# Performance work log

Measured on AMD Instinct MI355X. Metric: run time of the kernel, lower is better.

The kernel has to match this reference:

```python
import jax, jax.numpy as jnp
import numpy as np

B = 1024      # number of states
NP = 32       # SVGD particles per state
AD = 20       # act_dim
OD = 64       # obs_dim
H = 256       # critic hidden width
STEPS = 5     # num_svgd_steps
LR = 0.1      # svgd_lr (adaptive_lr disabled)
SP0 = 1.0     # svgd_sigma_p0
ALIM = 1.0    # act_limit


def _q(obs, X, w1, b1, w2, b2, w3, b3):
    h = jnp.concatenate([obs, X], axis=-1)
    h = jax.nn.relu(h @ w1 + b1)
    h = jax.nn.relu(h @ w2 + b2)
    return jnp.squeeze(h @ w3 + b3, -1)


def _rbf(X):
    # X: [B, NP, AD] -> K [B,NP,NP], diff [B,NP,NP,AD], gamma [B,1,1], K_grad [B,NP,NP,AD]
    diff = X[:, :, None, :] - X[:, None, :, :]
    dist_sq = jnp.sum(diff * diff, axis=-1)
    # adaptive bandwidth via median heuristic (adaptive_sig=True)
    med = jnp.median(dist_sq.reshape(dist_sq.shape[0], -1), axis=-1)
    sig_sq = med / (2.0 * jnp.log(NP + 1.0))
    gamma = (1.0 / (2.0 * sig_sq + 1e-8))[:, None, None]
    K = jnp.exp(-gamma * dist_sq)
    K_grad = -2.0 * gamma[..., None] * diff * K[..., None]  # d/dx_i K(x_i, x_j)
    return K, diff, gamma, K_grad


def setup_inputs():
    key = jax.random.key(0)
    ks = jax.random.split(key, 16)
    N = B * NP

    def lin(k, fi, fo):
        return (jax.random.normal(k, (fi, fo), jnp.float32) / np.sqrt(fi)).astype(jnp.float32)

    return {
        "obs": jax.random.normal(ks[0], (N, OD), jnp.float32),
        "a0": jax.random.normal(ks[1], (N, AD), jnp.float32) * np.sqrt(SP0),
        "q1_w1": lin(ks[2], OD + AD, H), "q1_b1": jnp.zeros((H,), jnp.float32),
        "q1_w2": lin(ks[3], H, H),       "q1_b2": jnp.zeros((H,), jnp.float32),
        "q1_w3": lin(ks[4], H, 1),       "q1_b3": jnp.zeros((1,), jnp.float32),
        "q2_w1": lin(ks[5], OD + AD, H), "q2_b1": jnp.zeros((H,), jnp.float32),
        "q2_w2": lin(ks[6], H, H),       "q2_b2": jnp.zeros((H,), jnp.float32),
        "q2_w3": lin(ks[7], H, 1),       "q2_b3": jnp.zeros((1,), jnp.float32),
    }


def reference(obs, a0, q1_w1, q1_b1, q1_w2, q1_b2, q1_w3, q1_b3,
              q2_w1, q2_b1, q2_w2, q2_b2, q2_w3, q2_b3):
    eye = jnp.eye(NP, dtype=a0.dtype)

    def q_min_sum(Xf):
        q1 = _q(obs, Xf, q1_w1, q1_b1, q1_w2, q1_b2, q1_w3, q1_b3)
        q2 = _q(obs, Xf, q2_w1, q2_b1, q2_w2, q2_b2, q2_w3, q2_b3)
        return jnp.sum(jnp.minimum(q1, q2))

    score_fn = jax.grad(q_min_sum)  # autograd score function

    def step(carry, _):
        a, logp = carry
        score = score_fn(a).reshape(-1, NP, AD)                 # [B,NP,AD]
        X = a.reshape(-1, NP, AD)
        K, diff, gamma, Kg = _rbf(X)
        phi = (jnp.einsum('bij,bjd->bid', K, score) + Kg.sum(axis=1)) / NP
        # log-prob correction terms (with_logprob=True)
        term1 = jnp.mean(jnp.sum(Kg * score[:, None, :, :], axis=-1), axis=2)     # [B,NP]
        inner = jnp.sum(jnp.transpose(Kg, (0, 2, 1, 3)) * diff, axis=-1) \
                - AD * (K - eye)
        term2 = -2.0 * gamma[:, :, 0] * jnp.mean(inner, axis=1)                   # [B,NP]
        logp = logp - LR * (term1 + term2)
        a = a + LR * phi.reshape(a.shape)                        # svgd_optim
        return (a, logp), None

    logp0 = jnp.zeros((B, NP), a0.dtype)
    (a, logp_svgd), _ = jax.lax.scan(step, (a0, logp0), None, length=STEPS)

    a_sq = ALIM * jnp.tanh(a)                                    # [B*NP, AD]
    logp_normal = (-AD * 0.5 * jnp.log(2.0 * jnp.pi * SP0)
                   - 0.5 / SP0 * jnp.sum(a0 * a0, axis=-1)).reshape(-1, NP)
    logp_tanh = -jnp.sum(2.0 * (jnp.log(2.0) - a - jax.nn.softplus(-2.0 * a)),
                         axis=-1).reshape(-1, NP)
    logp_a = jnp.mean(logp_normal + logp_svgd + logp_tanh, axis=-1)  # [B]
    return a_sq, logp_a
```

## Files before the change

### kernel.cpp

```cpp
#include <hip/hip_runtime.h>
#include <math.h>

#define NPART 32
#define ADIM  20
#define ODIM  64
#define HID   256
#define NSTEPS 5
#define LRC   0.1f
#define NBLK  512
#define LOG33 3.4965075614664802f

typedef short bf8 __attribute__((ext_vector_type(8)));
typedef float f4  __attribute__((ext_vector_type(4)));

#define OW1T(n) ((n)*24576)
#define OW2T(n) (49152 + (n)*65536)
#define OW2C(n) (180224 + (n)*65536)
#define OW1X(n) (311296 + (n)*8192)
#define OW3B(n) (327680 + (n)*256)
#define WS_ELEMS 328192

__device__ __forceinline__ short f2bf(float x) {
    unsigned u = __float_as_uint(x);
    u += 0x7FFFu + ((u >> 16) & 1u);
    return (short)(u >> 16);
}
__device__ __forceinline__ short f2bfT(float x) {
    return (short)(__float_as_uint(x) >> 16);
}
__device__ __forceinline__ float bf2f(short s) {
    return __uint_as_float(((unsigned)(unsigned short)s) << 16);
}

#define MFMA(a,b,c) __builtin_amdgcn_mfma_f32_16x16x32_bf16((a),(b),(c),0,0,0)

__global__ void prep_weights(const float* __restrict__ w1a, const float* __restrict__ w2a,
                             const float* __restrict__ w3a, const float* __restrict__ w1b,
                             const float* __restrict__ w2b, const float* __restrict__ w3b,
                             unsigned short* __restrict__ ws)
{
    int idx = blockIdx.x * 256 + threadIdx.x;
    if (idx >= WS_ELEMS) return;
    float val;
    if (idx < 49152) {
        int net = idx / 24576, rem = idx % 24576;
        int n = rem / 96, k = rem % 96;
        const float* w1 = net ? w1b : w1a;
        val = (k < 84) ? w1[k*256 + n] : 0.f;
    } else if (idx < 180224) {
        int t2 = idx - 49152; int net = t2 / 65536, rem = t2 % 65536;
        int n = rem / 256, k = rem % 256;
        const float* w2 = net ? w2b : w2a;
        val = w2[k*256 + n];
    } else if (idx < 311296) {
        int t2 = idx - 180224; int net = t2 / 65536, rem = t2 % 65536;
        const float* w2 = net ? w2b : w2a;
        val = w2[rem];
    } else if (idx < 327680) {
        int t2 = idx - 311296; int net = t2 / 8192, rem = t2 % 8192;
        int d = rem / 256, n = rem % 256;
        const float* w1 = net ? w1b : w1a;
        val = (d < 20) ? w1[(64 + d)*256 + n] : 0.f;
    } else {
        int t2 = idx - 327680; int net = t2 / 256, k = t2 % 256;
        const float* w3 = net ? w3b : w3a;
        val = w3[k];
    }
    ws[idx] = (unsigned short)f2bf(val);
}

__global__ void __launch_bounds__(512, 4)
svgd_main(const float* __restrict__ obs,  const float* __restrict__ a0g,
          const float* __restrict__ b1a,  const float* __restrict__ b2a, const float* __restrict__ b3a,
          const float* __restrict__ b1b,  const float* __restrict__ b2b, const float* __restrict__ b3b,
          const float* __restrict__ w3af, const float* __restrict__ w3bf,
          const unsigned short* __restrict__ ws, float* __restrict__ out)
{
    __shared__ __align__(16) short A0s[64*96];
    __shared__ __align__(16) short hbuf[64*264];
    __shared__ unsigned maskS[2][2][64][8];
    __shared__ float Xm[64*20];
    __shared__ float scoreS[64*21];
    __shared__ float qpart[2][8][64];
    __shared__ int   winsS[64];
    __shared__ float logps[64];
    __shared__ unsigned short lutI[496], lutJ[496];
    __shared__ float med2[4];
    __shared__ float qvS[64];
    __shared__ float normsS[64], diagS[64], rowKS[64];

    float* d2sF = (float*)hbuf;
    float* GSF  = ((float*)hbuf) + 2048;
    short* KbS  = hbuf + 8192;
    short* SBs  = hbuf + 10240;
    short* STbS = hbuf + 12288;
    short* XTbS = hbuf + 14336;

    const int t = threadIdx.x, b = blockIdx.x;
    const int lane = t & 63, wv = t >> 6;
    const int q = lane >> 4, mp = lane & 15;
    const int nb = wv * 32;

    for (int p = t; p < 64*ODIM; p += 512) {
        int i = p >> 6, d = p & 63;
        A0s[i*96 + d] = f2bfT(obs[(b*64 + i)*ODIM + d]);
    }
    for (int p = t; p < 64*ADIM; p += 512) {
        int i = p / 20, d = p - i*20;
        float v = a0g[(b*64 + i)*20 + d];
        Xm[p] = v;
        A0s[i*96 + 64 + d] = f2bfT(v);
    }
    for (int p = t; p < 64*12; p += 512) { int i = p/12, d = p - i*12; A0s[i*96 + 84 + d] = 0; }
    { unsigned* mz = &maskS[0][0][0][0];
      for (int p = t; p < 2*2*64*8; p += 512) mz[p] = 0u; }
    if (t < 496) {
        int i_ = 0, rem = t;
        while (rem >= 31 - i_) { rem -= 31 - i_; ++i_; }
        lutI[t] = (unsigned short)i_; lutJ[t] = (unsigned short)(i_ + 1 + rem);
    }
    if (t < 64) logps[t] = 0.f;
    __syncthreads();

    for (int step = 0; step < NSTEPS; ++step) {
        for (int net = 0; net < 2; ++net) {
            const unsigned short* w1t = ws + OW1T(net);
            const unsigned short* w2t = ws + OW2T(net);
            const float* b1p = net ? b1b : b1a;
            const float* b2p = net ? b2b : b2a;
            const float* w3p = net ? w3bf : w3af;

            f4 acc[4][2];
            #pragma unroll
            for (int h = 0; h < 4; ++h) { acc[h][0] = (f4){0,0,0,0}; acc[h][1] = (f4){0,0,0,0}; }
            {
                const unsigned short* bp0 = w1t + (size_t)(nb +      mp)*96 + q*8;
                const unsigned short* bp1 = w1t + (size_t)(nb + 16 + mp)*96 + q*8;
                bf8 bb0 = *(const bf8*)bp0, bb1 = *(const bf8*)bp1;
                #pragma unroll
                for (int k0 = 0; k0 < 96; k0 += 32) {
                    bf8 n0 = bb0, n1 = bb1;
                    if (k0 + 32 < 96) { n0 = *(const bf8*)(bp0 + k0 + 32); n1 = *(const bf8*)(bp1 + k0 + 32); }
                    #pragma unroll
                    for (int h = 0; h < 4; ++h) {
                        bf8 aa = *(const bf8*)&A0s[(h*16 + mp)*96 + k0 + q*8];
                        acc[h][0] = MFMA(aa, bb0, acc[h][0]);
                        acc[h][1] = MFMA(aa, bb1, acc[h][1]);
                    }
                    bb0 = n0; bb1 = n1;
                }
            }
            #pragma unroll
            for (int h = 0; h < 4; ++h) {
                #pragma unroll
                for (int s = 0; s < 2; ++s) {
                    int n0 = nb + s*16, col = n0 + mp;
                    float bias = b1p[col];
                    #pragma unroll
                    for (int r = 0; r < 4; ++r) {
                        float v = acc[h][s][r] + bias;
                        bool pos = v > 0.f;
                        unsigned long long bal = __ballot(pos);
                        hbuf[(h*16 + q*4 + r)*264 + col] = f2bfT(pos ? v : 0.f);
                        if (mp == 0)
                            atomicOr(&maskS[net][0][h*16 + q*4 + r][n0 >> 5],
                                     ((unsigned)((bal >> (q*16)) & 0xFFFFull)) << (n0 & 16));
                    }
                }
            }
            __syncthreads();

            #pragma unroll
            for (int h = 0; h < 4; ++h) { acc[h][0] = (f4){0,0,0,0}; acc[h][1] = (f4){0,0,0,0}; }
            {
                const unsigned short* bp0 = w2t + (size_t)(nb +      mp)*256 + q*8;
                const unsigned short* bp1 = w2t + (size_t)(nb + 16 + mp)*256 + q*8;
                bf8 bb0 = *(const bf8*)bp0, bb1 = *(const bf8*)bp1;
                #pragma unroll
                for (int k0 = 0; k0 < 256; k0 += 32) {
                    bf8 n0 = bb0, n1 = bb1;
                    if (k0 + 32 < 256) { n0 = *(const bf8*)(bp0 + k0 + 32); n1 = *(const bf8*)(bp1 + k0 + 32); }
                    #pragma unroll
                    for (int h = 0; h < 4; ++h) {
                        bf8 aa = *(const bf8*)&hbuf[(h*16 + mp)*264 + k0 + q*8];
                        acc[h][0] = MFMA(aa, bb0, acc[h][0]);
                        acc[h][1] = MFMA(aa, bb1, acc[h][1]);
                    }
                    bb0 = n0; bb1 = n1;
                }
            }
            {
                float qp[4][4] = {{0,0,0,0},{0,0,0,0},{0,0,0,0},{0,0,0,0}};
                #pragma unroll
                for (int h = 0; h < 4; ++h) {
                    #pragma unroll
                    for (int s = 0; s < 2; ++s) {
                        int n0 = nb + s*16, col = n0 + mp;
                        float bias = b2p[col], w3v = w3p[col];
                        #pragma unroll
                        for (int r = 0; r < 4; ++r) {
                            float v = acc[h][s][r] + bias;
                            bool pos = v > 0.f;
                            unsigned long long bal = __ballot(pos);
                            if (mp == 0)
                                atomicOr(&maskS[net][1][h*16 + q*4 + r][n0 >> 5],
                                         ((unsigned)((bal >> (q*16)) & 0xFFFFull)) << (n0 & 16));
                            qp[h][r] += pos ? v * w3v : 0.f;
                        }
                    }
                }
                #pragma unroll
                for (int d = 1; d < 16; d <<= 1)
                    #pragma unroll
                    for (int h = 0; h < 4; ++h)
                        #pragma unroll
                        for (int r = 0; r < 4; ++r)
                            qp[h][r] += __shfl_xor(qp[h][r], d, 64);
                if (mp == 0) {
                    #pragma unroll
                    for (int h = 0; h < 4; ++h)
                        #pragma unroll
                        for (int r = 0; r < 4; ++r)
                            qpart[net][wv][h*16 + q*4 + r] = qp[h][r];
                }
            }
            __syncthreads();
        }

        if (t < 64) {
            float q0 = b3a[0], q1 = b3b[0];
            #pragma unroll
            for (int w = 0; w < 8; ++w) { q0 += qpart[0][w][t]; q1 += qpart[1][w][t]; }
            winsS[t] = (q0 <= q1) ? 0 : 1;
        }
        __syncthreads();

        for (int net = 0; net < 2; ++net) {
            const unsigned short* w2c  = ws + OW2C(net);
            const unsigned short* w3b8 = ws + OW3B(net);

            f4 acc[4][2];
            #pragma unroll
            for (int h = 0; h < 4; ++h) { acc[h][0] = (f4){0,0,0,0}; acc[h][1] = (f4){0,0,0,0}; }
            int win[4];
            #pragma unroll
            for (int h = 0; h < 4; ++h) win[h] = (winsS[h*16 + mp] == net);
            {
                const unsigned short* bp0 = w2c + (size_t)(nb +      mp)*256 + q*8;
                const unsigned short* bp1 = w2c + (size_t)(nb + 16 + mp)*256 + q*8;
                bf8 bb0 = *(const bf8*)bp0, bb1 = *(const bf8*)bp1;
                #pragma unroll
                for (int k0 = 0; k0 < 256; k0 += 32) {
                    bf8 n0 = bb0, n1 = bb1;
                    if (k0 + 32 < 256) { n0 = *(const bf8*)(bp0 + k0 + 32); n1 = *(const bf8*)(bp1 + k0 + 32); }
                    bf8 w3v = *(const bf8*)(w3b8 + k0 + q*8);
                    #pragma unroll
                    for (int h = 0; h < 4; ++h) {
                        unsigned bits = win[h] ? ((maskS[net][1][h*16 + mp][k0 >> 5] >> (q*8)) & 0xFFu) : 0u;
                        bf8 aa;
                        #pragma unroll
                        for (int j = 0; j < 8; ++j)
                            aa[j] = ((bits >> j) & 1u) ? w3v[j] : (short)0;
                        acc[h][0] = MFMA(aa, bb0, acc[h][0]);
                        acc[h][1] = MFMA(aa, bb1, acc[h][1]);
                    }
                    bb0 = n0; bb1 = n1;
                }
            }
            #pragma unroll
            for (int h = 0; h < 4; ++h) {
                #pragma unroll
                for (int s = 0; s < 2; ++s) {
                    int col = nb + s*16 + mp;
                    #pragma unroll
                    for (int r = 0; r < 4; ++r) {
                        int row = h*16 + q*4 + r;
                        bool on = (maskS[net][0][row][col >> 5] >> (col & 31)) & 1u;
                        hbuf[row*264 + col] = f2bfT(on ? acc[h][s][r] : 0.f);
                    }
                }
            }
            __syncthreads();
            {
                int mt = wv & 3, ch = wv >> 2;
                const unsigned short* w1x = ws + OW1X(net);
                const unsigned short* bp  = w1x + (size_t)(ch*16 + mp)*256 + q*8;
                f4 sa = (f4){0,0,0,0};
                bf8 bx = *(const bf8*)bp;
                #pragma unroll
                for (int k0 = 0; k0 < 256; k0 += 32) {
                    bf8 nx = bx;
                    if (k0 + 32 < 256) nx = *(const bf8*)(bp + k0 + 32);
                    bf8 aa = *(const bf8*)&hbuf[(mt*16 + mp)*264 + k0 + q*8];
                    sa = MFMA(aa, bx, sa);
                    bx = nx;
                }
                int colD = ch*16 + mp;
                if (colD < 20) {
                    #pragma unroll
                    for (int r = 0; r < 4; ++r) {
                        int row = mt*16 + q*4 + r;
                        if (net == 0) scoreS[row*21 + colD]  = sa[r];
                        else          scoreS[row*21 + colD] += sa[r];
                    }
                }
            }
            __syncthreads();
        }

        if (t < 64) {
            int st = t >> 5;
            float nrm = 0.f, dg = 0.f;
            #pragma unroll
            for (int d = 0; d < 20; ++d) {
                float xb = bf2f(A0s[t*96 + 64 + d]);
                nrm += xb * xb;
                float sv = scoreS[t*21 + d];
                float xv = Xm[t*20 + d];
                dg += xv * sv;
                short sb = f2bfT(sv);
                SBs[t*32 + d] = sb;
                STbS[st*1024 + d*32 + (t & 31)] = sb;
                XTbS[st*1024 + d*32 + (t & 31)] = f2bfT(xv);
            }
            #pragma unroll
            for (int d = 20; d < 32; ++d) SBs[t*32 + d] = 0;
            normsS[t] = nrm;
            diagS[t]  = dg;
        }
        __syncthreads();

        {
            int stw = wv >> 2, mt = (wv >> 1) & 1, nt = wv & 1;
            bf8 aa  = *(const bf8*)&A0s[(stw*32 + mt*16 + mp)*96 + 64 + q*8];
            bf8 bbx = *(const bf8*)&A0s[(stw*32 + nt*16 + mp)*96 + 64 + q*8];
            bf8 bbs = *(const bf8*)&SBs[(stw*32 + nt*16 + mp)*32 + q*8];
            f4 gx = MFMA(aa, bbx, ((f4){0,0,0,0}));
            f4 gs = MFMA(aa, bbs, ((f4){0,0,0,0}));
            int jl = nt*16 + mp;
            float nj = normsS[stw*32 + jl];
            #pragma unroll
            for (int r = 0; r < 4; ++r) {
                int il = mt*16 + q*4 + r;
                d2sF[stw*1024 + il*32 + jl] = normsS[stw*32 + il] + nj - 2.f*gx[r];
                GSF [stw*1024 + il*32 + jl] = gs[r];
            }
        }
        __syncthreads();

        if (wv < 2) {
            const float* base = d2sF + wv*1024;
            float v[8];
            #pragma unroll
            for (int i = 0; i < 8; ++i) {
                int e = lane*8 + i;
                v[i] = (e < 496) ? base[lutI[e]*32 + lutJ[e]] : 3.4e38f;
            }
            for (int k = 2; k <= 512; k <<= 1) {
                for (int jj = k >> 1; jj >= 8; jj >>= 1) {
                    int lm = jj >> 3;
                    #pragma unroll
                    for (int i = 0; i < 8; ++i) {
                        float w = __shfl_xor(v[i], lm, 64);
                        int p = lane*8 + i;
                        bool takeMin = (((p & k) == 0) == ((p & jj) == 0));
                        v[i] = takeMin ? fminf(v[i], w) : fmaxf(v[i], w);
                    }
                }
                int jj0 = (k >> 1) < 4 ? (k >> 1) : 4;
                for (int jj = jj0; jj >= 1; jj >>= 1) {
                    #pragma unroll
                    for (int i = 0; i < 8; ++i) {
                        if ((i & jj) == 0) {
                            int i2 = i | jj;
                            int p = lane*8 + i;
                            bool up = ((p & k) == 0);
                            float x = v[i], y = v[i2];
                            float mn = fminf(x, y), mx = fmaxf(x, y);
                            v[i] = up ? mn : mx; v[i2] = up ? mx : mn;
                        }
                    }
                }
            }
            if (lane == 29) med2[wv*2 + 0] = v[7];
            if (lane == 30) med2[wv*2 + 1] = v[0];
        } else {
            unsigned* mz = &maskS[0][0][0][0];
            for (int p = t - 128; p < 2*2*64*8; p += 384) mz[p] = 0u;
        }
        __syncthreads();

        {
            int i = t >> 3, stw = i >> 5, il = i & 31, j0 = (t & 7) * 4;
            float medv = 0.5f * (med2[stw*2] + med2[stw*2 + 1]);
            float gam  = 1.f / (2.f * (medv / (2.f * LOG33)) + 1e-8f);
            float sK = 0.f, sKGS = 0.f, sKd2 = 0.f, sKdg = 0.f;
            #pragma unroll
            for (int jj = 0; jj < 4; ++jj) {
                int j = j0 + jj;
                float d2 = d2sF[stw*1024 + il*32 + j];
                float K  = expf(-gam * d2);
                KbS[stw*1024 + il*32 + j] = f2bfT(K);
                sK   += K;
                sKGS += K * GSF[stw*1024 + il*32 + j];
                sKd2 += K * d2;
                sKdg += K * diagS[stw*32 + j];
            }
            #pragma unroll
            for (int d = 1; d < 8; d <<= 1) {
                sK   += __shfl_xor(sK,   d, 64);
                sKGS += __shfl_xor(sKGS, d, 64);
                sKd2 += __shfl_xor(sKd2, d, 64);
                sKdg += __shfl_xor(sKdg, d, 64);
            }
            if ((t & 7) == 0) {
                rowKS[i] = sK;
                float sdots = sKGS - sKdg;
                float ssum  = -2.f*gam*sdots
                              - 2.f*gam*(2.f*gam*sKd2 - 20.f*(sK - 1.f));
                logps[i] -= LRC * (ssum * (1.f/32.f));
            }
        }
        __syncthreads();

        {
            int stw = wv >> 2, mt = (wv >> 1) & 1, nt = wv & 1;
            float medv = 0.5f * (med2[stw*2] + med2[stw*2 + 1]);
            float gam  = 1.f / (2.f * (medv / (2.f * LOG33)) + 1e-8f);
            bf8 aa  = *(const bf8*)&KbS [stw*1024 + (mt*16 + mp)*32 + q*8];
            bf8 b1v = *(const bf8*)&STbS[stw*1024 + (nt*16 + mp)*32 + q*8];
            bf8 b2v = *(const bf8*)&XTbS[stw*1024 + (nt*16 + mp)*32 + q*8];
            f4 ks = MFMA(aa, b1v, ((f4){0,0,0,0}));
            f4 kx = MFMA(aa, b2v, ((f4){0,0,0,0}));
            int dd = nt*16 + mp;
            if (dd < 20) {
                #pragma unroll
                for (int r = 0; r < 4; ++r) {
                    int gi = stw*32 + mt*16 + q*4 + r;
                    float xi  = Xm[gi*20 + dd];
                    float phi = (ks[r] + 2.f*gam*(xi*rowKS[gi] - kx[r])) * (1.f/32.f);
                    float nx  = xi + LRC * phi;
                    Xm[gi*20 + dd] = nx;
                    A0s[gi*96 + 64 + dd] = f2bfT(nx);
                }
            }
        }
        __syncthreads();
    }

    for (int p = t; p < 64*20; p += 512) {
        int i = p / 20, d = p - i*20;
        out[(b*64 + i)*20 + d] = tanhf(Xm[p]);
    }
    if (t < 64) {
        float lt = 0.f, s0 = 0.f;
        for (int d = 0; d < 20; ++d) {
            float a  = Xm[t*20 + d];
            float x  = -2.f * a;
            float sp = fmaxf(x, 0.f) + log1pf(expf(-fabsf(x)));
            lt -= 2.f * (0.69314718056f - a - sp);
            float v = a0g[(b*64 + t)*20 + d];
            s0 += v * v;
        }
        qvS[t] = -18.3787706641f - 0.5f*s0 + logps[t] + lt;
    }
    __syncthreads();
    if (t < 2) {
        float s = 0.f;
        for (int i = 0; i < 32; ++i) s += qvS[t*32 + i];
        out[1024*32*20 + b*2 + t] = s * (1.f/32.f);
    }
}

extern "C" void kernel_launch(void* const* d_in, const int* in_sizes, int n_in,
                              void* d_out, int out_size, void* d_ws, size_t ws_size,
                              hipStream_t stream) {
    unsigned short* ws = (unsigned short*)d_ws;
    prep_weights<<<(WS_ELEMS + 255)/256, 256, 0, stream>>>(
        (const float*)d_in[2],  (const float*)d_in[4],  (const float*)d_in[6],
        (const float*)d_in[8],  (const float*)d_in[10], (const float*)d_in[12], ws);
    svgd_main<<<NBLK, 512, 0, stream>>>(
        (const float*)d_in[0],  (const float*)d_in[1],
        (const float*)d_in[3],  (const float*)d_in[5],  (const float*)d_in[7],
        (const float*)d_in[9],  (const float*)d_in[11], (const float*)d_in[13],
        (const float*)d_in[6],  (const float*)d_in[12],
        ws, (float*)d_out);
}
```

Before: 497.5 us.

## Compute both critics' backward passes unconditionally and select score by min-Q winner

Each critic's backward pass now runs right after its forward pass. Masks are kept in registers instead of shared-memory atomicOr bitmasks. The ReLU mask of layer 2 times w3 is written directly as the A operand, and the two score results are held in registers and selected per row by which critic had the smaller Q. This removes the mask arrays, the ballot/atomic traffic and the scoreS/diagS buffers, and reads the diagonal from the GS matrix instead. In exchange it does the same MFMA work with extra register pressure for the saved accumulators. The weight prefetch double-buffering is dropped and occupancy is pinned via waves_per_eu.

```diff
diff --git a/kernel.cpp b/kernel.cpp
--- a/kernel.cpp
+++ b/kernel.cpp
@@ -69,7 +69,7 @@
     ws[idx] = (unsigned short)f2bf(val);
 }
 
-__global__ void __launch_bounds__(512, 4)
+__global__ void __launch_bounds__(512) __attribute__((amdgpu_waves_per_eu(4, 4)))
 svgd_main(const float* __restrict__ obs,  const float* __restrict__ a0g,
           const float* __restrict__ b1a,  const float* __restrict__ b2a, const float* __restrict__ b3a,
           const float* __restrict__ b1b,  const float* __restrict__ b2b, const float* __restrict__ b3b,
@@ -78,16 +78,14 @@
 {
     __shared__ __align__(16) short A0s[64*96];
     __shared__ __align__(16) short hbuf[64*264];
-    __shared__ unsigned maskS[2][2][64][8];
     __shared__ float Xm[64*20];
-    __shared__ float scoreS[64*21];
     __shared__ float qpart[2][8][64];
     __shared__ int   winsS[64];
     __shared__ float logps[64];
     __shared__ unsigned short lutI[496], lutJ[496];
     __shared__ float med2[4];
     __shared__ float qvS[64];
-    __shared__ float normsS[64], diagS[64], rowKS[64];
+    __shared__ float normsS[64], rowKS[64];
 
     float* d2sF = (float*)hbuf;
     float* GSF  = ((float*)hbuf) + 2048;
@@ -112,8 +110,6 @@
         A0s[i*96 + 64 + d] = f2bfT(v);
     }
     for (int p = t; p < 64*12; p += 512) { int i = p/12, d = p - i*12; A0s[i*96 + 84 + d] = 0; }
-    { unsigned* mz = &maskS[0][0][0][0];
-      for (int p = t; p < 2*2*64*8; p += 512) mz[p] = 0u; }
     if (t < 496) {
         int i_ = 0, rem = t;
         while (rem >= 31 - i_) { rem -= 31 - i_; ++i_; }
@@ -122,226 +118,211 @@
     if (t < 64) logps[t] = 0.f;
     __syncthreads();
 
+    const int mt = wv & 3, ch = wv >> 2;
+
     for (int step = 0; step < NSTEPS; ++step) {
+        f4 sav[2];
+
         for (int net = 0; net < 2; ++net) {
             const unsigned short* w1t = ws + OW1T(net);
             const unsigned short* w2t = ws + OW2T(net);
+            const unsigned short* w2c = ws + OW2C(net);
+            const unsigned short* w1x = ws + OW1X(net);
             const float* b1p = net ? b1b : b1a;
             const float* b2p = net ? b2b : b2a;
             const float* w3p = net ? w3bf : w3af;
-
-            f4 acc[4][2];
-            #pragma unroll
-            for (int h = 0; h < 4; ++h) { acc[h][0] = (f4){0,0,0,0}; acc[h][1] = (f4){0,0,0,0}; }
+            unsigned m0reg;
+
             {
-                const unsigned short* bp0 = w1t + (size_t)(nb +      mp)*96 + q*8;
-                const unsigned short* bp1 = w1t + (size_t)(nb + 16 + mp)*96 + q*8;
-                bf8 bb0 = *(const bf8*)bp0, bb1 = *(const bf8*)bp1;
+                f4 acc[4][2];
+                #pragma unroll
+                for (int h = 0; h < 4; ++h) { acc[h][0] = (f4){0,0,0,0}; acc[h][1] = (f4){0,0,0,0}; }
                 #pragma unroll
                 for (int k0 = 0; k0 < 96; k0 += 32) {
-                    bf8 n0 = bb0, n1 = bb1;
-                    if (k0 + 32 < 96) { n0 = *(const bf8*)(bp0 + k0 + 32); n1 = *(const bf8*)(bp1 + k0 + 32); }
+                    bf8 bb0 = *(const bf8*)(w1t + (size_t)(nb +      mp)*96 + k0 + q*8);
+                    bf8 bb1 = *(const bf8*)(w1t + (size_t)(nb + 16 + mp)*96 + k0 + q*8);
                     #pragma unroll
                     for (int h = 0; h < 4; ++h) {
                         bf8 aa = *(const bf8*)&A0s[(h*16 + mp)*96 + k0 + q*8];
                         acc[h][0] = MFMA(aa, bb0, acc[h][0]);
                         acc[h][1] = MFMA(aa, bb1, acc[h][1]);
                     }
-                    bb0 = n0; bb1 = n1;
-                }
-            }
-            #pragma unroll
-            for (int h = 0; h < 4; ++h) {
-                #pragma unroll
-                for (int s = 0; s < 2; ++s) {
-                    int n0 = nb + s*16, col = n0 + mp;
-                    float bias = b1p[col];
-                    #pragma unroll
-                    for (int r = 0; r < 4; ++r) {
-                        float v = acc[h][s][r] + bias;
-                        bool pos = v > 0.f;
-                        unsigned long long bal = __ballot(pos);
-                        hbuf[(h*16 + q*4 + r)*264 + col] = f2bfT(pos ? v : 0.f);
-                        if (mp == 0)
-                            atomicOr(&maskS[net][0][h*16 + q*4 + r][n0 >> 5],
-                                     ((unsigned)((bal >> (q*16)) & 0xFFFFull)) << (n0 & 16));
-                    }
-                }
+                }
+                unsigned mbits = 0u;
+                #pragma unroll
+                for (int h = 0; h < 4; ++h) {
+                    #pragma unroll
+                    for (int s = 0; s < 2; ++s) {
+                        int col = nb + s*16 + mp;
+                        float bias = b1p[col];
+                        #pragma unroll
+                        for (int r = 0; r < 4; ++r) {
+                            float v = acc[h][s][r] + bias;
+                            bool pos = v > 0.f;
+                            if (pos) mbits |= 1u << (h*8 + s*4 + r);
+                            hbuf[(h*16 + q*4 + r)*264 + col] = f2bfT(pos ? v : 0.f);
+                        }
+                    }
+                }
+                m0reg = mbits;
             }
             __syncthreads();
 
-            #pragma unroll
-            for (int h = 0; h < 4; ++h) { acc[h][0] = (f4){0,0,0,0}; acc[h][1] = (f4){0,0,0,0}; }
             {
-                const unsigned short* bp0 = w2t + (size_t)(nb +      mp)*256 + q*8;
-                const unsigned short* bp1 = w2t + (size_t)(nb + 16 + mp)*256 + q*8;
-                bf8 bb0 = *(const bf8*)bp0, bb1 = *(const bf8*)bp1;
+                f4 acc[4][2];
+                #pragma unroll
+                for (int h = 0; h < 4; ++h) { acc[h][0] = (f4){0,0,0,0}; acc[h][1] = (f4){0,0,0,0}; }
                 #pragma unroll
                 for (int k0 = 0; k0 < 256; k0 += 32) {
-                    bf8 n0 = bb0, n1 = bb1;
-                    if (k0 + 32 < 256) { n0 = *(const bf8*)(bp0 + k0 + 32); n1 = *(const bf8*)(bp1 + k0 + 32); }
+                    bf8 bb0 = *(const bf8*)(w2t + (size_t)(nb +      mp)*256 + k0 + q*8);
+                    bf8 bb1 = *(const bf8*)(w2t + (size_t)(nb + 16 + mp)*256 + k0 + q*8);
                     #pragma unroll
                     for (int h = 0; h < 4; ++h) {
                         bf8 aa = *(const bf8*)&hbuf[(h*16 + mp)*264 + k0 + q*8];
                         acc[h][0] = MFMA(aa, bb0, acc[h][0]);
                         acc[h][1] = MFMA(aa, bb1, acc[h][1]);
                     }
-                    bb0 = n0; bb1 = n1;
-                }
-            }
+                }
+                unsigned posreg = 0u;
+                {
+                    float qp[4][4] = {{0,0,0,0},{0,0,0,0},{0,0,0,0},{0,0,0,0}};
+                    #pragma unroll
+                    for (int h = 0; h < 4; ++h) {
+                        #pragma unroll
+                        for (int s = 0; s < 2; ++s) {
+                            int col = nb + s*16 + mp;
+                            float bias = b2p[col], w3v = w3p[col];
+                            #pragma unroll
+                            for (int r = 0; r < 4; ++r) {
+                                float v = acc[h][s][r] + bias;
+                                bool pos = v > 0.f;
+                                if (pos) posreg |= 1u << (h*8 + s*4 + r);
+                                qp[h][r] += pos ? v * w3v : 0.f;
+                            }
+                        }
+                    }
+                    #pragma unroll
+                    for (int d = 1; d < 16; d <<= 1)
+                        #pragma unroll
+                        for (int h = 0; h < 4; ++h)
+                            #pragma unroll
+                            for (int r = 0; r < 4; ++r)
+                                qp[h][r] += __shfl_xor(qp[h][r], d, 64);
+                    if (mp == 0) {
+                        #pragma unroll
+                        for (int h = 0; h < 4; ++h)
+                            #pragma unroll
+                            for (int r = 0; r < 4; ++r)
+                                qpart[net][wv][h*16 + q*4 + r] = qp[h][r];
+                    }
+                }
+                __syncthreads();
+                short w3s0 = (short)ws[OW3B(net) + nb + mp];
+                short w3s1 = (short)ws[OW3B(net) + nb + 16 + mp];
+                #pragma unroll
+                for (int h = 0; h < 4; ++h) {
+                    #pragma unroll
+                    for (int s = 0; s < 2; ++s) {
+                        int col = nb + s*16 + mp;
+                        short wv3 = s ? w3s1 : w3s0;
+                        #pragma unroll
+                        for (int r = 0; r < 4; ++r) {
+                            bool on = (posreg >> (h*8 + s*4 + r)) & 1u;
+                            hbuf[(h*16 + q*4 + r)*264 + col] = on ? wv3 : (short)0;
+                        }
+                    }
+                }
+                if (net == 1 && t < 64) {
+                    float q0 = b3a[0], q1 = b3b[0];
+                    #pragma unroll
+                    for (int w = 0; w < 8; ++w) { q0 += qpart[0][w][t]; q1 += qpart[1][w][t]; }
+                    winsS[t] = (q0 <= q1) ? 0 : 1;
+                }
+            }
+            __syncthreads();
+
             {
-                float qp[4][4] = {{0,0,0,0},{0,0,0,0},{0,0,0,0},{0,0,0,0}};
+                f4 accB[4][2];
+                #pragma unroll
+                for (int h = 0; h < 4; ++h) { accB[h][0] = (f4){0,0,0,0}; accB[h][1] = (f4){0,0,0,0}; }
+                #pragma unroll
+                for (int k0 = 0; k0 < 256; k0 += 32) {
+                    bf8 c0 = *(const bf8*)(w2c + (size_t)(nb +      mp)*256 + k0 + q*8);
+                    bf8 c1 = *(const bf8*)(w2c + (size_t)(nb + 16 + mp)*256 + k0 + q*8);
+                    #pragma unroll
+                    for (int h = 0; h < 4; ++h) {
+                        bf8 aa = *(const bf8*)&hbuf[(h*16 + mp)*264 + k0 + q*8];
+                        accB[h][0] = MFMA(aa, c0, accB[h][0]);
+                        accB[h][1] = MFMA(aa, c1, accB[h][1]);
+                    }
+                }
+                __syncthreads();
                 #pragma unroll
                 for (int h = 0; h < 4; ++h) {
                     #pragma unroll
                     for (int s = 0; s < 2; ++s) {
-                        int n0 = nb + s*16, col = n0 + mp;
-                        float bias = b2p[col], w3v = w3p[col];
+                        int col = nb + s*16 + mp;
                         #pragma unroll
                         for (int r = 0; r < 4; ++r) {
-                            float v = acc[h][s][r] + bias;
-                            bool pos = v > 0.f;
-                            unsigned long long bal = __ballot(pos);
-                            if (mp == 0)
-                                atomicOr(&maskS[net][1][h*16 + q*4 + r][n0 >> 5],
-                                         ((unsigned)((bal >> (q*16)) & 0xFFFFull)) << (n0 & 16));
-                            qp[h][r] += pos ? v * w3v : 0.f;
+                            bool on = (m0reg >> (h*8 + s*4 + r)) & 1u;
+                            hbuf[(h*16 + q*4 + r)*264 + col] = f2bfT(on ? accB[h][s][r] : 0.f);
                         }
                     }
                 }
-                #pragma unroll
-                for (int d = 1; d < 16; d <<= 1)
-                    #pragma unroll
-                    for (int h = 0; h < 4; ++h)
-                        #pragma unroll
-                        for (int r = 0; r < 4; ++r)
-                            qp[h][r] += __shfl_xor(qp[h][r], d, 64);
-                if (mp == 0) {
-                    #pragma unroll
-                    for (int h = 0; h < 4; ++h)
-                        #pragma unroll
-                        for (int r = 0; r < 4; ++r)
-                            qpart[net][wv][h*16 + q*4 + r] = qp[h][r];
-                }
             }
             __syncthreads();
-        }
-
-        if (t < 64) {
-            float q0 = b3a[0], q1 = b3b[0];
-            #pragma unroll
-            for (int w = 0; w < 8; ++w) { q0 += qpart[0][w][t]; q1 += qpart[1][w][t]; }
-            winsS[t] = (q0 <= q1) ? 0 : 1;
-        }
-        __syncthreads();
-
-        for (int net = 0; net < 2; ++net) {
-            const unsigned short* w2c  = ws + OW2C(net);
-            const unsigned short* w3b8 = ws + OW3B(net);
-
-            f4 acc[4][2];
-            #pragma unroll
-            for (int h = 0; h < 4; ++h) { acc[h][0] = (f4){0,0,0,0}; acc[h][1] = (f4){0,0,0,0}; }
-            int win[4];
-            #pragma unroll
-            for (int h = 0; h < 4; ++h) win[h] = (winsS[h*16 + mp] == net);
+
             {
-                const unsigned short* bp0 = w2c + (size_t)(nb +      mp)*256 + q*8;
-                const unsigned short* bp1 = w2c + (size_t)(nb + 16 + mp)*256 + q*8;
-                bf8 bb0 = *(const bf8*)bp0, bb1 = *(const bf8*)bp1;
+                f4 sa = (f4){0,0,0,0};
                 #pragma unroll
                 for (int k0 = 0; k0 < 256; k0 += 32) {
-                    bf8 n0 = bb0, n1 = bb1;
-                    if (k0 + 32 < 256) { n0 = *(const bf8*)(bp0 + k0 + 32); n1 = *(const bf8*)(bp1 + k0 + 32); }
-                    bf8 w3v = *(const bf8*)(w3b8 + k0 + q*8);
-                    #pragma unroll
-                    for (int h = 0; h < 4; ++h) {
-                        unsigned bits = win[h] ? ((maskS[net][1][h*16 + mp][k0 >> 5] >> (q*8)) & 0xFFu) : 0u;
-                        bf8 aa;
-                        #pragma unroll
-                        for (int j = 0; j < 8; ++j)
-                            aa[j] = ((bits >> j) & 1u) ? w3v[j] : (short)0;
-                        acc[h][0] = MFMA(aa, bb0, acc[h][0]);
-                        acc[h][1] = MFMA(aa, bb1, acc[h][1]);
-                    }
-                    bb0 = n0; bb1 = n1;
-                }
-            }
-            #pragma unroll
-            for (int h = 0; h < 4; ++h) {
-                #pragma unroll
-                for (int s = 0; s < 2; ++s) {
-                    int col = nb + s*16 + mp;
-                    #pragma unroll
-                    for (int r = 0; r < 4; ++r) {
-                        int row = h*16 + q*4 + r;
-                        bool on = (maskS[net][0][row][col >> 5] >> (col & 31)) & 1u;
-                        hbuf[row*264 + col] = f2bfT(on ? acc[h][s][r] : 0.f);
-                    }
-                }
-            }
-            __syncthreads();
-            {
-                int mt = wv & 3, ch = wv >> 2;
-                const unsigned short* w1x = ws + OW1X(net);
-                const unsigned short* bp  = w1x + (size_t)(ch*16 + mp)*256 + q*8;
-                f4 sa = (f4){0,0,0,0};
-                bf8 bx = *(const bf8*)bp;
-                #pragma unroll
-                for (int k0 = 0; k0 < 256; k0 += 32) {
-                    bf8 nx = bx;
-                    if (k0 + 32 < 256) nx = *(const bf8*)(bp + k0 + 32);
+                    bf8 bx = *(const bf8*)(w1x + (size_t)(ch*16 + mp)*256 + k0 + q*8);
                     bf8 aa = *(const bf8*)&hbuf[(mt*16 + mp)*264 + k0 + q*8];
                     sa = MFMA(aa, bx, sa);
-                    bx = nx;
-                }
-                int colD = ch*16 + mp;
-                if (colD < 20) {
-                    #pragma unroll
-                    for (int r = 0; r < 4; ++r) {
-                        int row = mt*16 + q*4 + r;
-                        if (net == 0) scoreS[row*21 + colD]  = sa[r];
-                        else          scoreS[row*21 + colD] += sa[r];
-                    }
-                }
+                }
+                sav[net] = sa;
             }
             __syncthreads();
         }
 
+        {
+            int colD = ch*16 + mp;
+            #pragma unroll
+            for (int r = 0; r < 4; ++r) {
+                int row = mt*16 + q*4 + r, st = row >> 5, il = row & 31;
+                float sv = winsS[row] ? sav[1][r] : sav[0][r];
+                short sb = f2bfT(sv);
+                SBs[row*32 + colD] = sb;
+                STbS[st*1024 + colD*32 + il] = sb;
+            }
+        }
         if (t < 64) {
-            int st = t >> 5;
-            float nrm = 0.f, dg = 0.f;
+            int st = t >> 5, il = t & 31;
+            float nrm = 0.f;
             #pragma unroll
             for (int d = 0; d < 20; ++d) {
                 float xb = bf2f(A0s[t*96 + 64 + d]);
                 nrm += xb * xb;
-                float sv = scoreS[t*21 + d];
-                float xv = Xm[t*20 + d];
-                dg += xv * sv;
-                short sb = f2bfT(sv);
-                SBs[t*32 + d] = sb;
-                STbS[st*1024 + d*32 + (t & 31)] = sb;
-                XTbS[st*1024 + d*32 + (t & 31)] = f2bfT(xv);
-            }
-            #pragma unroll
-            for (int d = 20; d < 32; ++d) SBs[t*32 + d] = 0;
+                XTbS[st*1024 + d*32 + il] = f2bfT(Xm[t*20 + d]);
+            }
+            #pragma unroll
+            for (int d = 20; d < 32; ++d) XTbS[st*1024 + d*32 + il] = 0;
             normsS[t] = nrm;
-            diagS[t]  = dg;
         }
         __syncthreads();
 
         {
-            int stw = wv >> 2, mt = (wv >> 1) & 1, nt = wv & 1;
-            bf8 aa  = *(const bf8*)&A0s[(stw*32 + mt*16 + mp)*96 + 64 + q*8];
-            bf8 bbx = *(const bf8*)&A0s[(stw*32 + nt*16 + mp)*96 + 64 + q*8];
-            bf8 bbs = *(const bf8*)&SBs[(stw*32 + nt*16 + mp)*32 + q*8];
+            int stw = wv >> 2, mtl = (wv >> 1) & 1, ntl = wv & 1;
+            bf8 aa  = *(const bf8*)&A0s[(stw*32 + mtl*16 + mp)*96 + 64 + q*8];
+            bf8 bbx = *(const bf8*)&A0s[(stw*32 + ntl*16 + mp)*96 + 64 + q*8];
+            bf8 bbs = *(const bf8*)&SBs[(stw*32 + ntl*16 + mp)*32 + q*8];
             f4 gx = MFMA(aa, bbx, ((f4){0,0,0,0}));
             f4 gs = MFMA(aa, bbs, ((f4){0,0,0,0}));
-            int jl = nt*16 + mp;
+            int jl = ntl*16 + mp;
             float nj = normsS[stw*32 + jl];
             #pragma unroll
             for (int r = 0; r < 4; ++r) {
-                int il = mt*16 + q*4 + r;
+                int il = mtl*16 + q*4 + r;
                 d2sF[stw*1024 + il*32 + jl] = normsS[stw*32 + il] + nj - 2.f*gx[r];
                 GSF [stw*1024 + il*32 + jl] = gs[r];
             }
@@ -384,9 +365,6 @@
             }
             if (lane == 29) med2[wv*2 + 0] = v[7];
             if (lane == 30) med2[wv*2 + 1] = v[0];
-        } else {
-            unsigned* mz = &maskS[0][0][0][0];
-            for (int p = t - 128; p < 2*2*64*8; p += 384) mz[p] = 0u;
         }
         __syncthreads();
 
@@ -404,7 +382,7 @@
                 sK   += K;
                 sKGS += K * GSF[stw*1024 + il*32 + j];
                 sKd2 += K * d2;
-                sKdg += K * diagS[stw*32 + j];
+                sKdg += K * GSF[stw*1024 + j*32 + j];
             }
             #pragma unroll
             for (int d = 1; d < 8; d <<= 1) {
@@ -424,19 +402,19 @@
         __syncthreads();
 
         {
-            int stw = wv >> 2, mt = (wv >> 1) & 1, nt = wv & 1;
+            int stw = wv >> 2, mtl = (wv >> 1) & 1, ntl = wv & 1;
             float medv = 0.5f * (med2[stw*2] + med2[stw*2 + 1]);
             float gam  = 1.f / (2.f * (medv / (2.f * LOG33)) + 1e-8f);
-            bf8 aa  = *(const bf8*)&KbS [stw*1024 + (mt*16 + mp)*32 + q*8];
-            bf8 b1v = *(const bf8*)&STbS[stw*1024 + (nt*16 + mp)*32 + q*8];
-            bf8 b2v = *(const bf8*)&XTbS[stw*1024 + (nt*16 + mp)*32 + q*8];
+            bf8 aa  = *(const bf8*)&KbS [stw*1024 + (mtl*16 + mp)*32 + q*8];
+            bf8 b1v = *(const bf8*)&STbS[stw*1024 + (ntl*16 + mp)*32 + q*8];
+            bf8 b2v = *(const bf8*)&XTbS[stw*1024 + (ntl*16 + mp)*32 + q*8];
             f4 ks = MFMA(aa, b1v, ((f4){0,0,0,0}));
             f4 kx = MFMA(aa, b2v, ((f4){0,0,0,0}));
-            int dd = nt*16 + mp;
+            int dd = ntl*16 + mp;
             if (dd < 20) {
                 #pragma unroll
                 for (int r = 0; r < 4; ++r) {
-                    int gi = stw*32 + mt*16 + q*4 + r;
+                    int gi = stw*32 + mtl*16 + q*4 + r;
                     float xi  = Xm[gi*20 + dd];
                     float phi = (ks[r] + 2.f*gam*(xi*rowKS[gi] - kx[r])) * (1.f/32.f);
                     float nx  = xi + LRC * phi;
```

Result: slower. 748.2 us (+50.4%).
